# Optimization experiments

Hardware: AMD Instinct MI355X
Metric: run time of the kernel (lower is better)

## Reference

```python
import jax, jax.numpy as jnp
import numpy as np

B = 16384
D = 128
NUM_CLASSES = 100


def setup_inputs() -> dict:
    key = jax.random.key(0)
    kx, kt = jax.random.split(key)
    x = jax.random.normal(kx, (B, D), dtype=jnp.float32)
    target = jax.random.randint(kt, (B,), 0, NUM_CLASSES, dtype=jnp.int64)
    return {"x": x, "target": target}


def reference(x, target):
    # Sum of pairwise Euclidean distances within each class, /2 (pair dedup), /batch.
    # Equivalent to the per-class loop: full BxB distance matrix masked to same-class pairs.
    batch_size = x.shape[0]
    sq_norms = jnp.sum(x * x, axis=-1)                       # [B]
    gram = x @ x.T                                           # [B, B]
    sq_dist = sq_norms[:, None] + sq_norms[None, :] - 2.0 * gram
    sq_dist = jnp.maximum(sq_dist, 0.0)
    same_class = target[:, None] == target[None, :]          # [B, B] bool
    off_diag = ~jnp.eye(batch_size, dtype=bool)
    mask = same_class & off_diag                             # diag distance is 0 anyway
    # masked sqrt to avoid sqrt of masked-out entries
    dist = jnp.where(mask, jnp.sqrt(jnp.where(mask, sq_dist, 1.0)), 0.0)
    distance_sum = jnp.sum(dist) / 2.0
    return distance_sum / batch_size
```

## Files before the change

kernel.cpp:

```cpp
#include <hip/hip_runtime.h>

#define B_SIZE 16384
#define DIM    128
#define NCLS   100
#define CAP    256
#define WAVES  8
#define BLK    512
#define SPANSZ (B_SIZE / WAVES)
#define WCAP   96

#define WS_PARTIAL 0

typedef short bf8 __attribute__((ext_vector_type(8)));
typedef float f32x4 __attribute__((ext_vector_type(4)));

__device__ __forceinline__ unsigned bf16_rne(float f) {
    unsigned u = __float_as_uint(f);
    return (u + 0x7FFFu + ((u >> 16) & 1u)) >> 16;
}

__global__ __launch_bounds__(BLK) void class_kernel(
        const float* __restrict__ x, const int* __restrict__ target,
        float* __restrict__ partials) {
    __shared__ __align__(16) unsigned short rows[CAP * DIM];
    __shared__ float nrm[CAP];
    __shared__ int   wreg[WAVES * WCAP];
    __shared__ int   wcnt[WAVES];
    __shared__ int   wbase[WAVES];
    __shared__ int   idxl[CAP];
    __shared__ int   n_sh;
    __shared__ float red[BLK];

    const int c    = blockIdx.x;
    const int tid  = threadIdx.x;
    const int w    = tid >> 6;
    const int lane = tid & 63;

    {
        int cnt = 0;
        const int base = w * SPANSZ;
        #pragma unroll 4
        for (int i = 0; i < SPANSZ; i += 64) {
            const int j = base + i + lane;
            const bool f = (target[j] == c);
            const unsigned long long m = __ballot(f);
            if (f) {
                const int p = cnt + __popcll(m & ((1ull << lane) - 1ull));
                if (p < WCAP) wreg[w * WCAP + p] = j;
            }
            cnt += __popcll(m);
        }
        if (lane == 0) wcnt[w] = (cnt < WCAP) ? cnt : WCAP;
    }
    __syncthreads();
    if (tid == 0) {
        int a = 0;
        for (int i = 0; i < WAVES; ++i) { wbase[i] = a; a += wcnt[i]; }
        n_sh = (a < CAP) ? a : CAP;
    }
    __syncthreads();
    const int n = n_sh;
    #pragma unroll
    for (int i = 0; i < WAVES; ++i) {
        if (tid < wcnt[i]) {
            const int dst = wbase[i] + tid;
            if (dst < CAP) idxl[dst] = wreg[i * WCAP + tid];
        }
    }
    __syncthreads();

    {
        const int grp = lane >> 4;
        const int ch  = lane & 15;
        for (int r = w * 4 + grp; r < n; r += 32) {
            const int idx = idxl[r];
            const float4 v0 = *reinterpret_cast<const float4*>(x + (size_t)idx * DIM + ch * 8);
            const float4 v1 = *reinterpret_cast<const float4*>(x + (size_t)idx * DIM + ch * 8 + 4);
            unsigned b0 = bf16_rne(v0.x), b1 = bf16_rne(v0.y),
                     b2 = bf16_rne(v0.z), b3 = bf16_rne(v0.w);
            unsigned b4 = bf16_rne(v1.x), b5 = bf16_rne(v1.y),
                     b6 = bf16_rne(v1.z), b7 = bf16_rne(v1.w);
            uint4 o;
            o.x = b0 | (b1 << 16); o.y = b2 | (b3 << 16);
            o.z = b4 | (b5 << 16); o.w = b6 | (b7 << 16);
            const int chunk = (r * 16 + ch) ^ (r & 7);
            *reinterpret_cast<uint4*>(&rows[chunk * 8]) = o;

            float c0 = __uint_as_float(b0 << 16), c1 = __uint_as_float(b1 << 16);
            float c2 = __uint_as_float(b2 << 16), c3 = __uint_as_float(b3 << 16);
            float c4 = __uint_as_float(b4 << 16), c5 = __uint_as_float(b5 << 16);
            float c6 = __uint_as_float(b6 << 16), c7 = __uint_as_float(b7 << 16);
            float s = c0*c0 + c1*c1 + c2*c2 + c3*c3 + c4*c4 + c5*c5 + c6*c6 + c7*c7;
            #pragma unroll
            for (int off = 1; off < 16; off <<= 1) s += __shfl_xor(s, off, 64);
            if (ch == 0) nrm[r] = s;
        }
    }
    __syncthreads();

    float acc = 0.0f;
    if (n > 0) {
        const int T  = (n + 31) >> 5;
        const int nt = T * (T + 1) / 2;
        const int r16 = lane & 15;
        const int kl  = lane >> 4;
        const int last = n - 1;

        for (int t = w; t < nt; t += WAVES) {
            int rem = t, ti = 0;
            while (rem >= T - ti) { rem -= T - ti; ++ti; }
            const int tj = ti + rem;
            const int pb = ti * 32, qb = tj * 32;

            const int pa0 = min(pb + r16, last), pa1 = min(pb + 16 + r16, last);
            const int qa0 = min(qb + r16, last), qa1 = min(qb + 16 + r16, last);

            f32x4 c00 = {0.f,0.f,0.f,0.f}, c01 = {0.f,0.f,0.f,0.f};
            f32x4 c10 = {0.f,0.f,0.f,0.f}, c11 = {0.f,0.f,0.f,0.f};
            #pragma unroll
            for (int ks = 0; ks < 4; ++ks) {
                const int kk = ks * 4 + kl;
                const bf8 a0 = *reinterpret_cast<const bf8*>(&rows[((pa0*16 + kk) ^ (pa0 & 7)) * 8]);
                const bf8 a1 = *reinterpret_cast<const bf8*>(&rows[((pa1*16 + kk) ^ (pa1 & 7)) * 8]);
                const bf8 b0 = *reinterpret_cast<const bf8*>(&rows[((qa0*16 + kk) ^ (qa0 & 7)) * 8]);
                const bf8 b1 = *reinterpret_cast<const bf8*>(&rows[((qa1*16 + kk) ^ (qa1 & 7)) * 8]);
                c00 = __builtin_amdgcn_mfma_f32_16x16x32_bf16(a0, b0, c00, 0, 0, 0);
                c01 = __builtin_amdgcn_mfma_f32_16x16x32_bf16(a0, b1, c01, 0, 0, 0);
                c10 = __builtin_amdgcn_mfma_f32_16x16x32_bf16(a1, b0, c10, 0, 0, 0);
                c11 = __builtin_amdgcn_mfma_f32_16x16x32_bf16(a1, b1, c11, 0, 0, 0);
            }

            const float nb0 = nrm[qa0];
            const float nb1 = nrm[qa1];
            float na[8];
            #pragma unroll
            for (int rg = 0; rg < 2; ++rg)
                #pragma unroll
                for (int r = 0; r < 4; ++r)
                    na[rg * 4 + r] = nrm[min(pb + rg * 16 + kl * 4 + r, last)];

            const bool diag = (ti == tj);
            #pragma unroll
            for (int sub = 0; sub < 4; ++sub) {
                const int rg = sub >> 1, cg = sub & 1;
                const f32x4 cc = (sub == 0) ? c00 : (sub == 1) ? c01 : (sub == 2) ? c10 : c11;
                const int qcol = cg * 16 + r16;
                const float nb = cg ? nb1 : nb0;
                #pragma unroll
                for (int r = 0; r < 4; ++r) {
                    const int prow = rg * 16 + kl * 4 + r;
                    const bool valid = (pb + prow < n) && (qb + qcol < n) &&
                                       (!diag || (prow < qcol));
                    if (valid) {
                        const float d2 = na[rg * 4 + r] + nb - 2.0f * cc[r];
                        acc += sqrtf(fmaxf(d2, 0.0f));
                    }
                }
            }
        }
    }

    red[tid] = acc;
    __syncthreads();
    for (int s = BLK / 2; s > 0; s >>= 1) {
        if (tid < s) red[tid] += red[tid + s];
        __syncthreads();
    }
    if (tid == 0) partials[c] = red[0];
}

__global__ void reduce_kernel(const float* __restrict__ partials, float* __restrict__ out) {
    const int lane = threadIdx.x;
    float a = (lane < NCLS) ? partials[lane] : 0.0f;
    if (lane + 64 < NCLS) a += partials[lane + 64];
    #pragma unroll
    for (int off = 1; off < 64; off <<= 1) a += __shfl_xor(a, off, 64);
    if (lane == 0) out[0] = a / (float)B_SIZE;
}

extern "C" void kernel_launch(void* const* d_in, const int* in_sizes, int n_in,
                              void* d_out, int out_size, void* d_ws, size_t ws_size,
                              hipStream_t stream) {
    const float* x      = (const float*)d_in[0];
    const int*   target = (const int*)d_in[1];
    float*       out    = (float*)d_out;
    float*       partials = (float*)((int*)d_ws + WS_PARTIAL);

    class_kernel<<<NCLS, BLK, 0, stream>>>(x, target, partials);
    reduce_kernel<<<1, 64, 0, stream>>>(partials, out);
}
```

Baseline: 22.11 us.

## Fuse final reduction into class kernel via cooperative grid sync

Merges the per-class kernel and the single-block final reduction into one cooperative launch, using a grid-wide barrier before block 0 sums the per-class partials. The block-level tree reduction over shared memory is also replaced by wave shuffles plus an 8-entry shared sum. This removes one kernel launch and the many __syncthreads of the tree reduction. In exchange it pays for a grid barrier and cooperative-launch overhead, and it requires all 100 blocks to be co-resident.

```diff
diff --git a/kernel.cpp b/kernel.cpp
--- a/kernel.cpp
+++ b/kernel.cpp
@@ -1,4 +1,7 @@
 #include <hip/hip_runtime.h>
+#include <hip/hip_cooperative_groups.h>
+
+namespace cg = cooperative_groups;
 
 #define B_SIZE 16384
 #define DIM    128
@@ -19,9 +22,9 @@
     return (u + 0x7FFFu + ((u >> 16) & 1u)) >> 16;
 }
 
-__global__ __launch_bounds__(BLK) void class_kernel(
+__global__ __launch_bounds__(BLK) void fused_kernel(
         const float* __restrict__ x, const int* __restrict__ target,
-        float* __restrict__ partials) {
+        float* __restrict__ partials, float* __restrict__ out) {
     __shared__ __align__(16) unsigned short rows[CAP * DIM];
     __shared__ float nrm[CAP];
     __shared__ int   wreg[WAVES * WCAP];
@@ -29,7 +32,7 @@
     __shared__ int   wbase[WAVES];
     __shared__ int   idxl[CAP];
     __shared__ int   n_sh;
-    __shared__ float red[BLK];
+    __shared__ float wsum[WAVES];
 
     const int c    = blockIdx.x;
     const int tid  = threadIdx.x;
@@ -160,22 +163,25 @@
         }
     }
 
-    red[tid] = acc;
+    #pragma unroll
+    for (int off = 1; off < 64; off <<= 1) acc += __shfl_xor(acc, off, 64);
+    if (lane == 0) wsum[w] = acc;
     __syncthreads();
-    for (int s = BLK / 2; s > 0; s >>= 1) {
-        if (tid < s) red[tid] += red[tid + s];
-        __syncthreads();
+    if (tid == 0) {
+        float s = 0.0f;
+        #pragma unroll
+        for (int i = 0; i < WAVES; ++i) s += wsum[i];
+        partials[c] = s;
     }
-    if (tid == 0) partials[c] = red[0];
-}
 
-__global__ void reduce_kernel(const float* __restrict__ partials, float* __restrict__ out) {
-    const int lane = threadIdx.x;
-    float a = (lane < NCLS) ? partials[lane] : 0.0f;
-    if (lane + 64 < NCLS) a += partials[lane + 64];
-    #pragma unroll
-    for (int off = 1; off < 64; off <<= 1) a += __shfl_xor(a, off, 64);
-    if (lane == 0) out[0] = a / (float)B_SIZE;
+    cg::this_grid().sync();
+    if (blockIdx.x == 0 && tid < 64) {
+        float a = (tid < NCLS) ? partials[tid] : 0.0f;
+        if (tid + 64 < NCLS) a += partials[tid + 64];
+        #pragma unroll
+        for (int off = 1; off < 64; off <<= 1) a += __shfl_xor(a, off, 64);
+        if (tid == 0) out[0] = a / (float)B_SIZE;
+    }
 }
 
 extern "C" void kernel_launch(void* const* d_in, const int* in_sizes, int n_in,
@@ -186,6 +192,7 @@
     float*       out    = (float*)d_out;
     float*       partials = (float*)((int*)d_ws + WS_PARTIAL);
 
-    class_kernel<<<NCLS, BLK, 0, stream>>>(x, target, partials);
-    reduce_kernel<<<1, 64, 0, stream>>>(partials, out);
+    void* args[] = { (void*)&x, (void*)&target, (void*)&partials, (void*)&out };
+    hipLaunchCooperativeKernel(reinterpret_cast<void*>(fused_kernel),
+                               dim3(NCLS), dim3(BLK), args, 0, stream);
 }
```

New measurement: 47.10 us. 2.13x slower.
